# Performance work log

Measured on AMD Instinct MI355X. Metric: run time of the kernel, lower is better.

The kernel has to match this reference:

```python
import jax, jax.numpy as jnp
import numpy as np

SPACE_DIM = 3
D = SPACE_DIM + 1            # (t, x, y, z)
D_MODEL = 1024
N_LAYERS = 4                 # hidden layers
N_MIX = 64
TRI = D * (D - 1) // 2       # strict upper-triangular entries of A
OUT_DIM = N_MIX * (TRI + 1)  # per-mixture triu values + mixture logits
TRIU_I, TRIU_J = np.triu_indices(D, k=1)
RHO_SCALE = 10.0


def setup_inputs() -> dict:
    key = jax.random.key(0)
    ks = jax.random.split(key, 8)
    B = 65536
    x = jax.random.normal(ks[0], (B, D), jnp.float32)
    W0 = jax.random.normal(ks[1], (D, D_MODEL), jnp.float32) * np.float32(np.sqrt(2.0 / D))
    b0 = jnp.zeros((D_MODEL,), jnp.float32)
    Wh = jax.random.normal(ks[2], (N_LAYERS, D_MODEL, D_MODEL), jnp.float32) * np.float32(np.sqrt(2.0 / D_MODEL))
    bh = jnp.zeros((N_LAYERS, D_MODEL), jnp.float32)
    Wout = jax.random.normal(ks[3], (D_MODEL, OUT_DIM), jnp.float32) * np.float32(np.sqrt(1.0 / D_MODEL))
    bout = jnp.zeros((OUT_DIM,), jnp.float32)
    return dict(x=x, W0=W0, b0=b0, Wh=Wh, bh=bh, Wout=Wout, bout=bout)


def _mlp(z, W0, b0, Wh, bh, Wout, bout):
    # z: (D,) -> (OUT_DIM,), swish MLP (NeuralConservationLaw backbone)
    h = jax.nn.silu(z @ W0 + b0)
    for l in range(N_LAYERS):  # fixed small layer count: python loop ok
        h = jax.nn.silu(h @ Wh[l] + bh[l])
    return h @ Wout + bout


def _A(z, params):
    # Antisymmetric matrix field A(z): mixture-weighted strict-upper-tri values.
    out = _mlp(z, *params)                              # (OUT_DIM,)
    logits = out[:N_MIX]                                # (N_MIX,)
    vals = out[N_MIX:].reshape(N_MIX, TRI)              # (N_MIX, TRI)
    a = jax.nn.softmax(logits) @ vals                   # (TRI,)
    A = jnp.zeros((D, D), out.dtype).at[TRIU_I, TRIU_J].set(a)
    return A - A.T                                      # antisymmetric (D, D)


def reference(x, W0, b0, Wh, bh, Wout, bout):
    params = (W0, b0, Wh, bh, Wout, bout)

    def u_single(z):
        # u_i = sum_j dA_ij/dz_j  (row-divergence of antisymmetric A => div u = 0)
        J = jax.jacfwd(lambda zz: _A(zz, params))(z)    # (D, D, D): J[i,j,k]=dA_ij/dz_k
        return jnp.einsum('ijj->i', J)                  # (D,)

    u = jax.vmap(u_single)(x)                           # (B, D)
    rho = u[..., :1] * RHO_SCALE
    flux = u[..., 1:]
    return jnp.concatenate([rho, flux], axis=-1)
```

## Files before the change

### kernel.cpp

```cpp
#include <hip/hip_runtime.h>
#include <hip/hip_bf16.h>

typedef _Float16 half8 __attribute__((ext_vector_type(8)));
typedef _Float16 half4 __attribute__((ext_vector_type(4)));
typedef float floatx4 __attribute__((ext_vector_type(4)));

__device__ __forceinline__ float bfu2f(unsigned short u) {
  return __uint_as_float(((unsigned)u) << 16);
}

__device__ __forceinline__ void gld16(const void* g, void* l) {
  __builtin_amdgcn_global_load_lds((const __attribute__((address_space(1))) void*)g,
                                   (__attribute__((address_space(3))) void*)l, 16, 0, 0);
}

__device__ __forceinline__ float fast_sig(float v) {
  return __builtin_amdgcn_rcpf(1.f + __expf(-v));
}

template <int NC>
__device__ __forceinline__ void xcd_decode(int lin, int NR, int& r, int& c) {
  if (NR & 7) {
    c = lin % NC;
    r = lin / NC;
  } else {
    int rl = lin & 7;
    int t = lin >> 3;
    c = t % NC;
    r = (t / NC) * 8 + rl;
  }
}

__global__ void probe_kernel(const unsigned short* __restrict__ w0, int* __restrict__ flag) {
  __shared__ int s;
  if (threadIdx.x == 0) s = 0;
  __syncthreads();
  int big = 0;
  for (int i = threadIdx.x; i < 2048; i += 256) {
    unsigned e = (w0[i] >> 7) & 0xFFu;
    if (e >= 134u) big = 1;
  }
  if (big) atomicOr(&s, 1);
  __syncthreads();
  if (threadIdx.x == 0) *flag = s;
}

__global__ void cvt_kernel(const void* __restrict__ in, _Float16* __restrict__ out, int nOut,
                           int nIn, const int* __restrict__ flag) {
  int i = blockIdx.x * 256 + threadIdx.x;
  if (i >= nOut) return;
  float v = 0.f;
  if (i < nIn) v = (*flag) ? ((const float*)in)[i] : bfu2f(((const unsigned short*)in)[i]);
  out[i] = (_Float16)v;
}

__global__ void tr_kernel(const void* __restrict__ in, _Float16* __restrict__ out, int Nin,
                          long inStride, long outStride, const int* __restrict__ flag) {
  __shared__ float tile[32][33];
  const int f = *flag;
  int k0 = blockIdx.x * 32, n0 = blockIdx.y * 32;
  long ib = (long)blockIdx.z * inStride;
  long ob = (long)blockIdx.z * outStride;
  int tx = threadIdx.x, ty = threadIdx.y;
#pragma unroll
  for (int i = 0; i < 4; i++) {
    int k = k0 + ty + i * 8, n = n0 + tx;
    float v = 0.f;
    if (n < Nin) {
      long idx = ib + (long)k * Nin + n;
      v = f ? ((const float*)in)[idx] : bfu2f(((const unsigned short*)in)[idx]);
    }
    tile[ty + i * 8][tx] = v;
  }
  __syncthreads();
#pragma unroll
  for (int i = 0; i < 4; i++) {
    int n = n0 + ty + i * 8, k = k0 + tx;
    out[ob + (long)n * 1024 + k] = (_Float16)tile[tx][ty + i * 8];
  }
}

__global__ __launch_bounds__(256)
void layer0_kernel(const _Float16* __restrict__ x16, const _Float16* __restrict__ W0c,
                   const _Float16* __restrict__ b0c, _Float16* __restrict__ H,
                   int chunkBase, int S1) {
  const int lb = blockIdx.x;
  const int t = threadIdx.x;
  const long gb = (long)chunkBase + lb;
  float z0 = (float)x16[gb * 4 + 0];
  float z1 = (float)x16[gb * 4 + 1];
  float z2 = (float)x16[gb * 4 + 2];
  float z3 = (float)x16[gb * 4 + 3];
  const int j0 = t * 4;
  float w[4][4];
#pragma unroll
  for (int i = 0; i < 4; i++) {
    half4 wv = *(const half4*)&W0c[i * 1024 + j0];
#pragma unroll
    for (int jj = 0; jj < 4; jj++) w[i][jj] = (float)wv[jj];
  }
  half4 o[5];
#pragma unroll
  for (int jj = 0; jj < 4; jj++) {
    float pre = z0 * w[0][jj] + z1 * w[1][jj] + z2 * w[2][jj] + z3 * w[3][jj] +
                (float)b0c[j0 + jj];
    float s = fast_sig(pre);
    o[0][jj] = (_Float16)(pre * s);
    float ds = s * (1.f + pre * (1.f - s));
    o[1][jj] = (_Float16)(ds * w[0][jj]);
    o[2][jj] = (_Float16)(ds * w[1][jj]);
    o[3][jj] = (_Float16)(ds * w[2][jj]);
    o[4][jj] = (_Float16)(ds * w[3][jj]);
  }
  long rowbase = (long)lb * 1024 + j0;
#pragma unroll
  for (int s = 0; s < 5; s++) *(half4*)&H[(long)s * S1 + rowbase] = o[s];
}

__global__ __launch_bounds__(256, 3)
void gemm_h1(const _Float16* __restrict__ A, const _Float16* __restrict__ Bt,
             const _Float16* __restrict__ bias, _Float16* __restrict__ C,
             _Float16* __restrict__ DS, int NR) {
  constexpr int K = 1024;
  __shared__ _Float16 SM[8192];
  _Float16* As = SM;
  _Float16* Bs = SM + 4096;
  _Float16* Ep = SM;
  const int tid = threadIdx.x;
  const int wave = tid >> 6;
  const int lane = tid & 63;
  int rb, cb;
  xcd_decode<8>(blockIdx.x, NR, rb, cb);
  const int n0 = cb * 128;
  const long m0 = (long)rb * 128;

  const int srow0 = (wave * 2 + 0) * 16 + (lane >> 2);
  const int srow1 = (wave * 2 + 1) * 16 + (lane >> 2);
  const int scol = (lane & 3) * 8;
  const _Float16* gA0 = A + (m0 + srow0) * K + scol;
  const _Float16* gA1 = A + (m0 + srow1) * K + scol;
  const _Float16* gB0 = Bt + (long)(n0 + srow0) * K + scol;
  const _Float16* gB1 = Bt + (long)(n0 + srow1) * K + scol;
  _Float16* lA0 = As + (wave * 2 + 0) * 512;
  _Float16* lA1 = As + (wave * 2 + 1) * 512;
  _Float16* lB0 = Bs + (wave * 2 + 0) * 512;
  _Float16* lB1 = Bs + (wave * 2 + 1) * 512;

  const int wm = (wave & 1) * 64;
  const int wn = (wave >> 1) * 64;
  const int fr = lane & 15;
  const int fc = (lane >> 4) * 8;
  const int c0f = lane & 15;
  const int rqk = lane >> 4;
  const int myRound = wave & 1;

  float bv[4];
#pragma unroll
  for (int ni = 0; ni < 4; ni++) bv[ni] = (float)bias[n0 + wn + ni * 16 + c0f];

  const int erow = tid >> 4;
  const int ecol = (tid & 15) * 8;
  const int ecolp = ecol ^ (wave << 4);

  floatx4 acc[4][4];
#pragma unroll
  for (int i = 0; i < 4; i++)
#pragma unroll
    for (int j = 0; j < 4; j++) acc[i][j] = (floatx4)(0.f);

  for (int kk = 0; kk < K; kk += 32) {
    __syncthreads();
    gld16(gA0 + kk, lA0);
    gld16(gA1 + kk, lA1);
    gld16(gB0 + kk, lB0);
    gld16(gB1 + kk, lB1);
    __syncthreads();
    half8 af[4], bf[4];
#pragma unroll
    for (int i = 0; i < 4; i++) af[i] = *(const half8*)&As[(wm + i * 16 + fr) * 32 + fc];
#pragma unroll
    for (int i = 0; i < 4; i++) bf[i] = *(const half8*)&Bs[(wn + i * 16 + fr) * 32 + fc];
#pragma unroll
    for (int mi = 0; mi < 4; mi++)
#pragma unroll
      for (int ni = 0; ni < 4; ni++)
        acc[mi][ni] = __builtin_amdgcn_mfma_f32_16x16x32_f16(af[mi], bf[ni], acc[mi][ni], 0, 0, 0);
  }

#pragma unroll
  for (int r = 0; r < 2; r++) {
    __syncthreads();
    if (myRound == r) {
#pragma unroll
      for (int mi = 0; mi < 4; mi++)
#pragma unroll
        for (int ni = 0; ni < 4; ni++) {
          int colp = (wn + ni * 16 + c0f) ^ (rqk << 4);
#pragma unroll
          for (int rr = 0; rr < 4; rr++) {
            int row_local = mi * 16 + rqk * 4 + rr;
            Ep[row_local * 128 + colp] = (_Float16)(acc[mi][ni][rr] + bv[ni]);
          }
        }
    }
    __syncthreads();
#pragma unroll
    for (int p = 0; p < 4; p++) {
      int row_local = p * 16 + erow;
      half8 vv = *(const half8*)&Ep[row_local * 128 + ecolp];
      long row = m0 + r * 64 + row_local;
      half8 hv, dv;
#pragma unroll
      for (int e = 0; e < 8; e++) {
        float xv = (float)vv[e];
        float sg = fast_sig(xv);
        hv[e] = (_Float16)(xv * sg);
        dv[e] = (_Float16)(sg * (1.f + xv * (1.f - sg)));
      }
      *(half8*)&C[row * (long)K + n0 + ecol] = hv;
      *(half8*)&DS[row * (long)K + n0 + ecol] = dv;
    }
  }
}

__global__ __launch_bounds__(256, 3)
void gemm_h2(const _Float16* __restrict__ A, const _Float16* __restrict__ Bt,
             _Float16* __restrict__ C, const _Float16* __restrict__ DS, int bcMask, int NR) {
  constexpr int K = 1024;
  __shared__ _Float16 SM[24576];
  _Float16* Ep = SM;
  const int tid = threadIdx.x;
  const int wave = tid >> 6;
  const int lane = tid & 63;
  int rb, cb;
  xcd_decode<8>(blockIdx.x, NR, rb, cb);
  const int n0 = cb * 128;
  const long m0 = (long)rb * 128;

  const int srow0 = (wave * 2 + 0) * 16 + (lane >> 2);
  const int srow1 = (wave * 2 + 1) * 16 + (lane >> 2);
  const int scol = (((lane & 3) ^ ((lane >> 3) & 3))) * 8;
  const _Float16* gA0 = A + (m0 + srow0) * K + scol;
  const _Float16* gA1 = A + (m0 + srow1) * K + scol;
  const _Float16* gB0 = Bt + (long)(n0 + srow0) * K + scol;
  const _Float16* gB1 = Bt + (long)(n0 + srow1) * K + scol;
  const int loffA0 = (wave * 2 + 0) * 512;
  const int loffA1 = (wave * 2 + 1) * 512;

  const int wm = (wave & 1) * 64;
  const int wn = (wave >> 1) * 64;
  const int fr = lane & 15;
  const int fc = (((lane >> 4) ^ ((lane >> 1) & 3))) * 8;
  const int c0f = lane & 15;
  const int rqk = lane >> 4;
  const int myRound = wave & 1;

  const int erow = tid >> 4;
  const int ecol = (tid & 15) * 8;
  const int ecolp = ecol ^ (wave << 4);

  floatx4 acc[4][4];
#pragma unroll
  for (int i = 0; i < 4; i++)
#pragma unroll
    for (int j = 0; j < 4; j++) acc[i][j] = (floatx4)(0.f);

  {
    _Float16* b0p = SM;
    gld16(gA0 + 0, b0p + loffA0);
    gld16(gA1 + 0, b0p + loffA1);
    gld16(gB0 + 0, b0p + 4096 + loffA0);
    gld16(gB1 + 0, b0p + 4096 + loffA1);
    _Float16* b1p = SM + 8192;
    gld16(gA0 + 32, b1p + loffA0);
    gld16(gA1 + 32, b1p + loffA1);
    gld16(gB0 + 32, b1p + 4096 + loffA0);
    gld16(gB1 + 32, b1p + 4096 + loffA1);
  }

  int bufCur = 0;
  int bufNxt = 2;
  for (int it = 0; it < 32; ++it) {
    if (it < 31) __builtin_amdgcn_s_waitcnt(0x0F74);
    else         __builtin_amdgcn_s_waitcnt(0x0F70);
    __builtin_amdgcn_s_barrier();
    if (it < 30) {
      const int kk = (it + 2) * 32;
      _Float16* bp = SM + bufNxt * 8192;
      gld16(gA0 + kk, bp + loffA0);
      gld16(gA1 + kk, bp + loffA1);
      gld16(gB0 + kk, bp + 4096 + loffA0);
      gld16(gB1 + kk, bp + 4096 + loffA1);
    }
    const _Float16* Asb = SM + bufCur * 8192;
    const _Float16* Bsb = Asb + 4096;
    half8 af[4], bf[4];
#pragma unroll
    for (int i = 0; i < 4; i++) af[i] = *(const half8*)&Asb[(wm + i * 16 + fr) * 32 + fc];
#pragma unroll
    for (int i = 0; i < 4; i++) bf[i] = *(const half8*)&Bsb[(wn + i * 16 + fr) * 32 + fc];
#pragma unroll
    for (int mi = 0; mi < 4; mi++)
#pragma unroll
      for (int ni = 0; ni < 4; ni++)
        acc[mi][ni] = __builtin_amdgcn_mfma_f32_16x16x32_f16(af[mi], bf[ni], acc[mi][ni], 0, 0, 0);
    bufCur = (bufCur == 2) ? 0 : bufCur + 1;
    bufNxt = (bufNxt == 2) ? 0 : bufNxt + 1;
  }

#pragma unroll
  for (int r = 0; r < 2; r++) {
    __syncthreads();
    if (myRound == r) {
#pragma unroll
      for (int mi = 0; mi < 4; mi++)
#pragma unroll
        for (int ni = 0; ni < 4; ni++) {
          int colp = (wn + ni * 16 + c0f) ^ (rqk << 4);
#pragma unroll
          for (int rr = 0; rr < 4; rr++) {
            int row_local = mi * 16 + rqk * 4 + rr;
            Ep[row_local * 128 + colp] = (_Float16)acc[mi][ni][rr];
          }
        }
    }
    __syncthreads();
#pragma unroll
    for (int p = 0; p < 4; p++) {
      int row_local = p * 16 + erow;
      half8 vv = *(const half8*)&Ep[row_local * 128 + ecolp];
      long row = m0 + r * 64 + row_local;
      half8 dv = *(const half8*)&DS[(long)(row & bcMask) * K + n0 + ecol];
      *(half8*)&C[row * (long)K + n0 + ecol] = dv * vv;
    }
  }
}

__global__ __launch_bounds__(256, 4)
void gemm_out(const _Float16* __restrict__ A, const _Float16* __restrict__ Bt,
              const _Float16* __restrict__ bias, _Float16* __restrict__ C,
              int Nreal, int ldc, int biasRows, int NR) {
  constexpr int K = 1024;
  __shared__ _Float16 SM[8192];
  _Float16* As = SM;
  _Float16* Bs = SM + 4096;
  _Float16* Ep = SM;
  const int tid = threadIdx.x;
  const int wave = tid >> 6;
  const int lane = tid & 63;
  int rb, cb;
  xcd_decode<4>(blockIdx.x, NR, rb, cb);
  const int n0 = cb * 128;
  const long m0 = (long)rb * 128;

  const int srow0 = (wave * 2 + 0) * 16 + (lane >> 2);
  const int srow1 = (wave * 2 + 1) * 16 + (lane >> 2);
  const int scol = (lane & 3) * 8;
  const _Float16* gA0 = A + (m0 + srow0) * K + scol;
  const _Float16* gA1 = A + (m0 + srow1) * K + scol;
  const _Float16* gB0 = Bt + (long)(n0 + srow0) * K + scol;
  const _Float16* gB1 = Bt + (long)(n0 + srow1) * K + scol;
  _Float16* lA0 = As + (wave * 2 + 0) * 512;
  _Float16* lA1 = As + (wave * 2 + 1) * 512;
  _Float16* lB0 = Bs + (wave * 2 + 0) * 512;
  _Float16* lB1 = Bs + (wave * 2 + 1) * 512;

  const int wm = (wave & 1) * 64;
  const int wn = (wave >> 1) * 64;
  const int fr = lane & 15;
  const int fc = (lane >> 4) * 8;
  const int c0f = lane & 15;
  const int rqk = lane >> 4;
  const int myRound = wave & 1;

  float bv[4];
#pragma unroll
  for (int ni = 0; ni < 4; ni++) bv[ni] = (float)bias[n0 + wn + ni * 16 + c0f];

  const int erow = tid >> 4;
  const int ecol = (tid & 15) * 8;
  const int ecolp = ecol ^ (wave << 4);

  floatx4 acc[4][4];
#pragma unroll
  for (int i = 0; i < 4; i++)
#pragma unroll
    for (int j = 0; j < 4; j++) acc[i][j] = (floatx4)(0.f);

  for (int kk = 0; kk < K; kk += 32) {
    __syncthreads();
    gld16(gA0 + kk, lA0);
    gld16(gA1 + kk, lA1);
    gld16(gB0 + kk, lB0);
    gld16(gB1 + kk, lB1);
    __syncthreads();
    half8 af[4], bf[4];
#pragma unroll
    for (int i = 0; i < 4; i++) af[i] = *(const half8*)&As[(wm + i * 16 + fr) * 32 + fc];
#pragma unroll
    for (int i = 0; i < 4; i++) bf[i] = *(const half8*)&Bs[(wn + i * 16 + fr) * 32 + fc];
#pragma unroll
    for (int mi = 0; mi < 4; mi++)
#pragma unroll
      for (int ni = 0; ni < 4; ni++)
        acc[mi][ni] = __builtin_amdgcn_mfma_f32_16x16x32_f16(af[mi], bf[ni], acc[mi][ni], 0, 0, 0);
  }

#pragma unroll
  for (int r = 0; r < 2; r++) {
    __syncthreads();
    if (myRound == r) {
#pragma unroll
      for (int mi = 0; mi < 4; mi++)
#pragma unroll
        for (int ni = 0; ni < 4; ni++) {
          int colp = (wn + ni * 16 + c0f) ^ (rqk << 4);
#pragma unroll
          for (int rr = 0; rr < 4; rr++) {
            int row_local = mi * 16 + rqk * 4 + rr;
            long grow = m0 + wm + mi * 16 + rqk * 4 + rr;
            float v = acc[mi][ni][rr] + (grow < biasRows ? bv[ni] : 0.f);
            Ep[row_local * 128 + colp] = (_Float16)v;
          }
        }
    }
    __syncthreads();
#pragma unroll
    for (int p = 0; p < 4; p++) {
      int row_local = p * 16 + erow;
      int col = n0 + ecol;
      if (col < Nreal) {
        half8 vv = *(const half8*)&Ep[row_local * 128 + ecolp];
        long row = m0 + r * 64 + row_local;
        *(half8*)&C[row * (long)ldc + col] = vv;
      }
    }
  }
}

__global__ __launch_bounds__(256)
void finalize_kernel(const _Float16* __restrict__ O5, void* __restrict__ outp,
                     int chunkBase, int Bc, const int* __restrict__ flag) {
  const int wid = threadIdx.x >> 6;
  const int lane = threadIdx.x & 63;
  const int lb = blockIdx.x * 4 + wid;
  const long SO = (long)Bc * 448;
  const long base0 = (long)lb * 448;

  union UU { unsigned u; _Float16 h[2]; };

  float lg = (float)O5[base0 + lane];
  float vals[6];
  {
    const unsigned* vp = (const unsigned*)(O5 + base0 + 64 + lane * 6);
#pragma unroll
    for (int q = 0; q < 3; q++) {
      UU c; c.u = vp[q];
      vals[2 * q] = (float)c.h[0];
      vals[2 * q + 1] = (float)c.h[1];
    }
  }
  float dl[4], dv[4][6];
#pragma unroll
  for (int t = 0; t < 4; t++) {
    long bs = (long)(1 + t) * SO + base0;
    dl[t] = (float)O5[bs + lane];
    const unsigned* vp = (const unsigned*)(O5 + bs + 64 + lane * 6);
#pragma unroll
    for (int q = 0; q < 3; q++) {
      UU c; c.u = vp[q];
      dv[t][2 * q] = (float)c.h[0];
      dv[t][2 * q + 1] = (float)c.h[1];
    }
  }
  float mx = lg;
#pragma unroll
  for (int off = 32; off >= 1; off >>= 1) mx = fmaxf(mx, __shfl_xor(mx, off));
  float e = __expf(lg - mx);
  float S = e;
#pragma unroll
  for (int off = 32; off >= 1; off >>= 1) S += __shfl_xor(S, off);
  float pv = e / S;
  float st[4];
#pragma unroll
  for (int t = 0; t < 4; t++) {
    float v = pv * dl[t];
#pragma unroll
    for (int off = 32; off >= 1; off >>= 1) v += __shfl_xor(v, off);
    st[t] = v;
  }
  float da[4][6];
#pragma unroll
  for (int t = 0; t < 4; t++) {
    float w = pv * (dl[t] - st[t]);
#pragma unroll
    for (int k = 0; k < 6; k++) {
      float v = w * vals[k] + pv * dv[t][k];
#pragma unroll
      for (int off = 32; off >= 1; off >>= 1) v += __shfl_xor(v, off);
      da[t][k] = v;
    }
  }
  if (lane == 0) {
    float u0 = da[1][0] + da[2][1] + da[3][2];
    float u1 = -da[0][0] + da[2][3] + da[3][4];
    float u2 = -da[0][1] - da[1][3] + da[3][5];
    float u3 = -da[0][2] - da[1][4] - da[2][5];
    long ob = (long)(chunkBase + lb) * 4;
    if (*flag) {
      float* o = (float*)outp;
      o[ob] = 10.f * u0; o[ob + 1] = u1; o[ob + 2] = u2; o[ob + 3] = u3;
    } else {
      __hip_bfloat16* o = (__hip_bfloat16*)outp;
      o[ob] = __float2bfloat16(10.f * u0);
      o[ob + 1] = __float2bfloat16(u1);
      o[ob + 2] = __float2bfloat16(u2);
      o[ob + 3] = __float2bfloat16(u3);
    }
  }
}

extern "C" void kernel_launch(void* const* d_in, const int* in_sizes, int n_in,
                              void* d_out, int out_size, void* d_ws, size_t ws_size,
                              hipStream_t stream) {
  const void* x = d_in[0];
  const void* W0 = d_in[1];
  const void* b0 = d_in[2];
  const void* Wh = d_in[3];
  const void* bh = d_in[4];
  const void* Wout = d_in[5];
  const void* bout = d_in[6];
  const int B = in_sizes[0] / 4;

  char* p = (char*)d_ws;
  int* flag = (int*)p;                 p += 256;
  _Float16* W0c = (_Float16*)p;        p += 4096 * 2;
  _Float16* b0c = (_Float16*)p;        p += 1024 * 2;
  _Float16* bhc = (_Float16*)p;        p += 4096 * 2;
  _Float16* boutc = (_Float16*)p;      p += 512 * 2;
  p += 256 - ((size_t)(p - (char*)d_ws) & 255);
  _Float16* x16 = (_Float16*)p;        p += (size_t)B * 4 * 2;
  _Float16* WhT = (_Float16*)p;        p += (size_t)4 * 1024 * 1024 * 2;
  _Float16* WoutT = (_Float16*)p;      p += (size_t)512 * 1024 * 2;
  size_t used = (size_t)(p - (char*)d_ws);
  size_t rem = (ws_size > used) ? (ws_size - used) : 0;
  const size_t perS = 10240 + 10240 + 2048 + 4480;
  long bcap = (long)(rem / perS);
  int Bc = 128;
  while ((long)Bc * 2 <= bcap && Bc * 2 <= B) Bc *= 2;
  _Float16* Ha = (_Float16*)p;         p += (size_t)5 * Bc * 1024 * 2;
  _Float16* Hb = (_Float16*)p;         p += (size_t)5 * Bc * 1024 * 2;
  _Float16* DS = (_Float16*)p;         p += (size_t)Bc * 1024 * 2;
  _Float16* PREo = (_Float16*)p;

  probe_kernel<<<1, 256, 0, stream>>>((const unsigned short*)W0, flag);
  cvt_kernel<<<(B * 4 + 255) / 256, 256, 0, stream>>>(x, x16, B * 4, B * 4, flag);
  cvt_kernel<<<16, 256, 0, stream>>>(W0, W0c, 4096, 4096, flag);
  cvt_kernel<<<4, 256, 0, stream>>>(b0, b0c, 1024, 1024, flag);
  cvt_kernel<<<16, 256, 0, stream>>>(bh, bhc, 4096, 4096, flag);
  cvt_kernel<<<2, 256, 0, stream>>>(bout, boutc, 512, 448, flag);
  tr_kernel<<<dim3(32, 32, 4), dim3(32, 8), 0, stream>>>(Wh, WhT, 1024, 1024L * 1024, 1024L * 1024, flag);
  tr_kernel<<<dim3(32, 16, 1), dim3(32, 8), 0, stream>>>(Wout, WoutT, 448, 0L, 0L, flag);

  const int nChunks = B / Bc;
  for (int c = 0; c < nChunks; c++) {
    const int base = c * Bc;
    const int S1 = Bc * 1024;
    _Float16* Hin = Ha;
    _Float16* Hout = Hb;
    layer0_kernel<<<Bc, 256, 0, stream>>>(x16, W0c, b0c, Hin, base, S1);
    const int NR1 = Bc / 128;
    const int NR2 = 4 * Bc / 128;
    const int NRo = 5 * Bc / 128;
    for (int l = 0; l < 4; l++) {
      const _Float16* Wl = WhT + (size_t)l * 1024 * 1024;
      gemm_h1<<<8 * NR1, 256, 0, stream>>>(
          Hin, Wl, bhc + l * 1024, Hout, DS, NR1);
      gemm_h2<<<8 * NR2, 256, 0, stream>>>(
          Hin + S1, Wl, Hout + S1, DS, Bc - 1, NR2);
      _Float16* t = Hin; Hin = Hout; Hout = t;
    }
    gemm_out<<<4 * NRo, 256, 0, stream>>>(
        Hin, WoutT, boutc, PREo, 448, 448, Bc, NRo);
    finalize_kernel<<<Bc / 4, 256, 0, stream>>>(PREo, d_out, base, Bc, flag);
  }
}
```

Before: 4.569 ms.

## Enlarge gemm_h2 tile to 256x256 with 8 waves and split B-load phases

The tangent-propagation GEMM moves from 128x128 tiles with 4 waves to 256x256 tiles with 8 waves (512 threads), each wave computing 128x64. This cuts global and LDS traffic per FLOP. The B-tile prefetch is split across two half-iterations around an extra barrier, and the MFMA bursts are wrapped in s_setprio. The epilogue is rewritten for four 64-row rounds over a 256-wide staging buffer. In exchange it uses more registers and 96KB of LDS per block, which limits occupancy, and produces fewer blocks for load balance.

Result: faster. 3.922 ms (-14.2%).

```diff
diff --git a/kernel.cpp b/kernel.cpp
--- a/kernel.cpp
+++ b/kernel.cpp
@@ -223,59 +223,52 @@
   }
 }
 
-__global__ __launch_bounds__(256, 3)
+__global__ __launch_bounds__(512, 2)
 void gemm_h2(const _Float16* __restrict__ A, const _Float16* __restrict__ Bt,
              _Float16* __restrict__ C, const _Float16* __restrict__ DS, int bcMask, int NR) {
   constexpr int K = 1024;
-  __shared__ _Float16 SM[24576];
-  _Float16* Ep = SM;
+  __shared__ _Float16 SM[49152];
   const int tid = threadIdx.x;
   const int wave = tid >> 6;
   const int lane = tid & 63;
   int rb, cb;
-  xcd_decode<8>(blockIdx.x, NR, rb, cb);
-  const int n0 = cb * 128;
-  const long m0 = (long)rb * 128;
-
-  const int srow0 = (wave * 2 + 0) * 16 + (lane >> 2);
-  const int srow1 = (wave * 2 + 1) * 16 + (lane >> 2);
-  const int scol = (((lane & 3) ^ ((lane >> 3) & 3))) * 8;
-  const _Float16* gA0 = A + (m0 + srow0) * K + scol;
-  const _Float16* gA1 = A + (m0 + srow1) * K + scol;
-  const _Float16* gB0 = Bt + (long)(n0 + srow0) * K + scol;
-  const _Float16* gB1 = Bt + (long)(n0 + srow1) * K + scol;
-  const int loffA0 = (wave * 2 + 0) * 512;
-  const int loffA1 = (wave * 2 + 1) * 512;
-
-  const int wm = (wave & 1) * 64;
-  const int wn = (wave >> 1) * 64;
+  xcd_decode<4>(blockIdx.x, NR, rb, cb);
+  const long m0 = (long)rb * 256;
+  const int n0 = cb * 256;
+
+  const int srow = wave * 32 + (lane >> 2);
+  const int scol = ((lane & 3) ^ ((lane >> 3) & 3)) * 8;
+  const _Float16* gA0 = A + (m0 + srow) * K + scol;
+  const _Float16* gA1 = gA0 + 16 * K;
+  const _Float16* gB0 = Bt + (long)(n0 + srow) * K + scol;
+  const _Float16* gB1 = gB0 + 16 * K;
+  const int loff0 = wave * 1024;
+  const int loff1 = loff0 + 512;
+
+  const int wr = wave >> 2;
+  const int wc = wave & 3;
   const int fr = lane & 15;
-  const int fc = (((lane >> 4) ^ ((lane >> 1) & 3))) * 8;
+  const int fc = ((lane >> 4) ^ ((lane >> 1) & 3)) * 8;
+  const int rqk = lane >> 4;
   const int c0f = lane & 15;
-  const int rqk = lane >> 4;
-  const int myRound = wave & 1;
-
-  const int erow = tid >> 4;
-  const int ecol = (tid & 15) * 8;
-  const int ecolp = ecol ^ (wave << 4);
-
-  floatx4 acc[4][4];
-#pragma unroll
-  for (int i = 0; i < 4; i++)
+
+  floatx4 acc[8][4];
+#pragma unroll
+  for (int i = 0; i < 8; i++)
 #pragma unroll
     for (int j = 0; j < 4; j++) acc[i][j] = (floatx4)(0.f);
 
   {
     _Float16* b0p = SM;
-    gld16(gA0 + 0, b0p + loffA0);
-    gld16(gA1 + 0, b0p + loffA1);
-    gld16(gB0 + 0, b0p + 4096 + loffA0);
-    gld16(gB1 + 0, b0p + 4096 + loffA1);
-    _Float16* b1p = SM + 8192;
-    gld16(gA0 + 32, b1p + loffA0);
-    gld16(gA1 + 32, b1p + loffA1);
-    gld16(gB0 + 32, b1p + 4096 + loffA0);
-    gld16(gB1 + 32, b1p + 4096 + loffA1);
+    gld16(gA0 + 0, b0p + loff0);
+    gld16(gA1 + 0, b0p + loff1);
+    gld16(gB0 + 0, b0p + 8192 + loff0);
+    gld16(gB1 + 0, b0p + 8192 + loff1);
+    _Float16* b1p = SM + 16384;
+    gld16(gA0 + 32, b1p + loff0);
+    gld16(gA1 + 32, b1p + loff1);
+    gld16(gB0 + 32, b1p + 8192 + loff0);
+    gld16(gB1 + 32, b1p + 8192 + loff1);
   }
 
   int bufCur = 0;
@@ -284,54 +277,75 @@
     if (it < 31) __builtin_amdgcn_s_waitcnt(0x0F74);
     else         __builtin_amdgcn_s_waitcnt(0x0F70);
     __builtin_amdgcn_s_barrier();
+    const int kk = (it + 2) * 32;
+    _Float16* bp = SM + bufNxt * 16384;
     if (it < 30) {
-      const int kk = (it + 2) * 32;
-      _Float16* bp = SM + bufNxt * 8192;
-      gld16(gA0 + kk, bp + loffA0);
-      gld16(gA1 + kk, bp + loffA1);
-      gld16(gB0 + kk, bp + 4096 + loffA0);
-      gld16(gB1 + kk, bp + 4096 + loffA1);
-    }
-    const _Float16* Asb = SM + bufCur * 8192;
-    const _Float16* Bsb = Asb + 4096;
-    half8 af[4], bf[4];
-#pragma unroll
-    for (int i = 0; i < 4; i++) af[i] = *(const half8*)&Asb[(wm + i * 16 + fr) * 32 + fc];
-#pragma unroll
-    for (int i = 0; i < 4; i++) bf[i] = *(const half8*)&Bsb[(wn + i * 16 + fr) * 32 + fc];
-#pragma unroll
-    for (int mi = 0; mi < 4; mi++)
-#pragma unroll
-      for (int ni = 0; ni < 4; ni++)
-        acc[mi][ni] = __builtin_amdgcn_mfma_f32_16x16x32_f16(af[mi], bf[ni], acc[mi][ni], 0, 0, 0);
+      gld16(gA0 + kk, bp + loff0);
+      gld16(gA1 + kk, bp + loff1);
+    }
+    const _Float16* Asb = SM + bufCur * 16384;
+    const _Float16* Bsb = Asb + 8192;
+    half8 af[8], bf0, bf1, bf2, bf3;
+#pragma unroll
+    for (int i = 0; i < 8; i++)
+      af[i] = *(const half8*)&Asb[(wr * 128 + i * 16 + fr) * 32 + fc];
+    bf0 = *(const half8*)&Bsb[(wc * 64 + 0 * 16 + fr) * 32 + fc];
+    bf1 = *(const half8*)&Bsb[(wc * 64 + 1 * 16 + fr) * 32 + fc];
+    __builtin_amdgcn_s_setprio(1);
+#pragma unroll
+    for (int mi = 0; mi < 8; mi++) {
+      acc[mi][0] = __builtin_amdgcn_mfma_f32_16x16x32_f16(af[mi], bf0, acc[mi][0], 0, 0, 0);
+      acc[mi][1] = __builtin_amdgcn_mfma_f32_16x16x32_f16(af[mi], bf1, acc[mi][1], 0, 0, 0);
+    }
+    __builtin_amdgcn_s_setprio(0);
+    __builtin_amdgcn_s_barrier();
+    if (it < 30) {
+      gld16(gB0 + kk, bp + 8192 + loff0);
+      gld16(gB1 + kk, bp + 8192 + loff1);
+    }
+    bf2 = *(const half8*)&Bsb[(wc * 64 + 2 * 16 + fr) * 32 + fc];
+    bf3 = *(const half8*)&Bsb[(wc * 64 + 3 * 16 + fr) * 32 + fc];
+    __builtin_amdgcn_s_setprio(1);
+#pragma unroll
+    for (int mi = 0; mi < 8; mi++) {
+      acc[mi][2] = __builtin_amdgcn_mfma_f32_16x16x32_f16(af[mi], bf2, acc[mi][2], 0, 0, 0);
+      acc[mi][3] = __builtin_amdgcn_mfma_f32_16x16x32_f16(af[mi], bf3, acc[mi][3], 0, 0, 0);
+    }
+    __builtin_amdgcn_s_setprio(0);
     bufCur = (bufCur == 2) ? 0 : bufCur + 1;
     bufNxt = (bufNxt == 2) ? 0 : bufNxt + 1;
   }
 
-#pragma unroll
-  for (int r = 0; r < 2; r++) {
-    __syncthreads();
-    if (myRound == r) {
-#pragma unroll
-      for (int mi = 0; mi < 4; mi++)
-#pragma unroll
-        for (int ni = 0; ni < 4; ni++) {
-          int colp = (wn + ni * 16 + c0f) ^ (rqk << 4);
-#pragma unroll
-          for (int rr = 0; rr < 4; rr++) {
-            int row_local = mi * 16 + rqk * 4 + rr;
-            Ep[row_local * 128 + colp] = (_Float16)acc[mi][ni][rr];
+  const int erow = tid >> 3;
+  const int rqkr = (erow >> 2) & 3;
+#pragma unroll
+  for (int r = 0; r < 4; ++r) {
+    __syncthreads();
+    if (wr == (r >> 1)) {
+      const int mib = (r & 1) * 4;
+#pragma unroll
+      for (int mi2 = 0; mi2 < 4; ++mi2) {
+#pragma unroll
+        for (int ni = 0; ni < 4; ++ni) {
+          int colp = (wc * 64 + ni * 16 + c0f) ^ (rqk << 4);
+#pragma unroll
+          for (int rr = 0; rr < 4; ++rr) {
+            int row_local = mi2 * 16 + rqk * 4 + rr;
+            SM[row_local * 256 + colp] = (_Float16)acc[mib + mi2][ni][rr];
           }
         }
-    }
-    __syncthreads();
-#pragma unroll
-    for (int p = 0; p < 4; p++) {
-      int row_local = p * 16 + erow;
-      half8 vv = *(const half8*)&Ep[row_local * 128 + ecolp];
-      long row = m0 + r * 64 + row_local;
-      half8 dv = *(const half8*)&DS[(long)(row & bcMask) * K + n0 + ecol];
-      *(half8*)&C[row * (long)K + n0 + ecol] = dv * vv;
+      }
+    }
+    __syncthreads();
+    long grow = m0 + r * 64 + erow;
+    long dsrow = grow & bcMask;
+#pragma unroll
+    for (int q = 0; q < 4; ++q) {
+      int col = (tid & 7) * 8 + q * 64;
+      int colp = col ^ (rqkr << 4);
+      half8 vv = *(const half8*)&SM[erow * 256 + colp];
+      half8 dv = *(const half8*)&DS[dsrow * (long)K + n0 + col];
+      *(half8*)&C[grow * (long)K + n0 + col] = dv * vv;
     }
   }
 }
@@ -570,14 +584,14 @@
     _Float16* Hout = Hb;
     layer0_kernel<<<Bc, 256, 0, stream>>>(x16, W0c, b0c, Hin, base, S1);
     const int NR1 = Bc / 128;
-    const int NR2 = 4 * Bc / 128;
+    const int NR2row = Bc / 64;
     const int NRo = 5 * Bc / 128;
     for (int l = 0; l < 4; l++) {
       const _Float16* Wl = WhT + (size_t)l * 1024 * 1024;
       gemm_h1<<<8 * NR1, 256, 0, stream>>>(
           Hin, Wl, bhc + l * 1024, Hout, DS, NR1);
-      gemm_h2<<<8 * NR2, 256, 0, stream>>>(
-          Hin + S1, Wl, Hout + S1, DS, Bc - 1, NR2);
+      gemm_h2<<<4 * NR2row, 512, 0, stream>>>(
+          Hin + S1, Wl, Hout + S1, DS, Bc - 1, NR2row);
       _Float16* t = Hin; Hin = Hout; Hout = t;
     }
     gemm_out<<<4 * NRo, 256, 0, stream>>>(
```
